# Kernel optimization log

Hardware: AMD Instinct MI355X
Metric: run time of the kernel (lower is better)

Reference implementation:

```python
import jax, jax.numpy as jnp
import numpy as np

EPS = 1e-3  # jitter to guarantee SPD input

def setup_inputs() -> dict:
    key = jax.random.key(0)
    B, N = 8192, 64
    a = jax.random.normal(key, (B, N, N), dtype=jnp.float32)
    # build batched SPD matrices: x = A A^T / N + eps I
    x = jnp.einsum('bij,bkj->bik', a, a) / N + EPS * jnp.eye(N, dtype=jnp.float32)
    return {"x": x}

def reference(x) -> jnp.ndarray:
    # LogEig: eigendecompose each SPD matrix, take log of eigenvalues,
    # reconstruct: U diag(log s) U^T
    w, v = jnp.linalg.eigh(x)                       # w: [B,N], v: [B,N,N]
    logw = jnp.log(w)
    # (v * logw[..., None, :]) scales columns of v by log-eigenvalues
    out = jnp.einsum('bik,bk,bjk->bij', v, logw, v)
    return out
```

## Files before the change

### kernel.cpp

```cpp
#include <hip/hip_runtime.h>
#include <math.h>

#define NTHR   512
#define SWEEPS 7

__device__ __forceinline__ int ring_next_even(int s) {
    return (s == 0) ? 0 : ((s == 62) ? 63 : s + 2);
}
__device__ __forceinline__ int ring_next_odd(int s) {
    return (s == 1) ? 2 : s - 2;
}
__device__ __forceinline__ int cpos(int c) {
    return (c >> 1) + ((c & 1) << 5);
}

__global__ __launch_bounds__(NTHR, 8)
void logeig_jacobi(const float* __restrict__ x, float* __restrict__ out) {
    __shared__ float A[64 * 64];
    __shared__ float Vt[64 * 64];
    __shared__ __align__(16) float2 prm[32];
    __shared__ float logw[64];

    const int tid = threadIdx.x;
    const int w   = tid >> 6;
    const int lan = tid & 63;
    const int J   = tid & 31;
    const int bit = (lan >> 5) & 1;
    const int base = 4 * w + bit;
    const int kv  = tid >> 4;
    const int cch = tid & 15;

    const int wpP = cpos(ring_next_even(2 * J));
    const int wpQ = cpos(ring_next_odd(2 * J + 1));

    const size_t base_el = (size_t)blockIdx.x * 4096;

    {
        const float4* x4 = (const float4*)(x + base_el);
        for (int idx4 = tid; idx4 < 1024; idx4 += NTHR) {
            int i = idx4 >> 4, t = idx4 & 15;
            float4 v = x4[idx4];
            *(float2*)&A[i * 64 + 2 * t]      = make_float2(v.x, v.z);
            *(float2*)&A[i * 64 + 32 + 2 * t] = make_float2(v.y, v.w);
            float4 id;
            id.x = (4 * t + 0 == i) ? 1.0f : 0.0f;
            id.y = (4 * t + 1 == i) ? 1.0f : 0.0f;
            id.z = (4 * t + 2 == i) ? 1.0f : 0.0f;
            id.w = (4 * t + 3 == i) ? 1.0f : 0.0f;
            ((float4*)Vt)[idx4] = id;
        }
    }
    __syncthreads();

    for (int sweep = 0; sweep < SWEEPS; ++sweep) {
        for (int r = 0; r < 63; ++r) {
            if (tid < 32) {
                int k = tid;
                float app = A[(2 * k) * 64 + k];
                float apq = A[(2 * k) * 64 + k + 32];
                float aqq = A[(2 * k + 1) * 64 + k + 32];
                float c = 1.0f, s = 0.0f;
                if (apq != 0.0f) {
                    float tau = (aqq - app) / (2.0f * apq);
                    float t   = copysignf(1.0f, tau) /
                                (fabsf(tau) + sqrtf(1.0f + tau * tau));
                    c = 1.0f / sqrtf(1.0f + t * t);
                    s = t * c;
                }
                prm[k] = make_float2(c, s);
            }

            float4 ablk[2];
            #pragma unroll
            for (int k = 0; k < 2; ++k) {
                int r0 = (2 * (base + 2 * k)) * 64;
                int r1 = r0 + 64;
                ablk[k] = make_float4(A[r0 + J], A[r0 + J + 32],
                                      A[r1 + J], A[r1 + J + 32]);
            }
            float4 vtop = *(const float4*)&Vt[(2 * kv) * 64 + 4 * cch];
            float4 vbot = *(const float4*)&Vt[(2 * kv + 1) * 64 + 4 * cch];
            __syncthreads();

            float2 pJ = prm[J];
            float2 pV = prm[kv];
            float2 pI[2];
            pI[0] = prm[base];
            pI[1] = prm[base + 2];

            #pragma unroll
            for (int k = 0; k < 2; ++k) {
                float cI = pI[k].x, sI = pI[k].y;
                float cJ = pJ.x,   sJ = pJ.y;
                float m00 = ablk[k].x, m01 = ablk[k].y;
                float m10 = ablk[k].z, m11 = ablk[k].w;
                float t00 = cI * m00 - sI * m10, t01 = cI * m01 - sI * m11;
                float t10 = sI * m00 + cI * m10, t11 = sI * m01 + cI * m11;
                float n00 = cJ * t00 - sJ * t01, n01 = sJ * t00 + cJ * t01;
                float n10 = cJ * t10 - sJ * t11, n11 = sJ * t10 + cJ * t11;
                int I  = base + 2 * k;
                int dPr = ring_next_even(2 * I) * 64;
                int dQr = ring_next_odd(2 * I + 1) * 64;
                A[dPr + wpP] = n00;
                A[dPr + wpQ] = n01;
                A[dQr + wpP] = n10;
                A[dQr + wpQ] = n11;
            }

            {
                float cV = pV.x, sV = pV.y;
                int dPr = ring_next_even(2 * kv);
                int dQr = ring_next_odd(2 * kv + 1);
                float4 n0, n1;
                n0.x = cV * vtop.x - sV * vbot.x;  n1.x = sV * vtop.x + cV * vbot.x;
                n0.y = cV * vtop.y - sV * vbot.y;  n1.y = sV * vtop.y + cV * vbot.y;
                n0.z = cV * vtop.z - sV * vbot.z;  n1.z = sV * vtop.z + cV * vbot.z;
                n0.w = cV * vtop.w - sV * vbot.w;  n1.w = sV * vtop.w + cV * vbot.w;
                *(float4*)&Vt[dPr * 64 + 4 * cch] = n0;
                *(float4*)&Vt[dQr * 64 + 4 * cch] = n1;
            }
            __syncthreads();
        }
    }

    if (tid < 64) {
        int p = (tid >> 1) + ((tid & 1) << 5);
        logw[tid] = logf(A[tid * 64 + p]);
    }
    __syncthreads();

    for (int idx4 = tid; idx4 < 1024; idx4 += NTHR) {
        int k = idx4 >> 4;
        float lw = logw[k];
        float4 v = ((float4*)Vt)[idx4];
        v.x *= lw; v.y *= lw; v.z *= lw; v.w *= lw;
        ((float4*)A)[idx4] = v;
    }
    __syncthreads();

    float4* out4 = (float4*)(out + base_el);
    for (int idx4 = tid; idx4 < 1024; idx4 += NTHR) {
        int i = idx4 >> 4, j4 = idx4 & 15;
        float4 acc = make_float4(0.0f, 0.0f, 0.0f, 0.0f);
        #pragma unroll 8
        for (int k = 0; k < 64; ++k) {
            float a = A[k * 64 + i];
            float4 vv = ((float4*)Vt)[k * 16 + j4];
            acc.x += a * vv.x; acc.y += a * vv.y;
            acc.z += a * vv.z; acc.w += a * vv.w;
        }
        out4[idx4] = acc;
    }
}

extern "C" void kernel_launch(void* const* d_in, const int* in_sizes, int n_in,
                              void* d_out, int out_size, void* d_ws, size_t ws_size,
                              hipStream_t stream) {
    const float* x = (const float*)d_in[0];
    float* o = (float*)d_out;
    int B = in_sizes[0] / 4096;
    logeig_jacobi<<<B, NTHR, 0, stream>>>(x, o);
}
```

Before: 5.044 ms.

## Exploit symmetry in Jacobi A update, computing only upper-triangle 2x2 blocks

Each thread now owns one off-diagonal 2x2 block pair (k,q) and writes both it and its transpose, cutting the A-rotation work per sweep step roughly in half (one block per thread instead of two). The diagonal blocks are written directly in closed form (app - t*apq, 0, 0, aqq + t*apq) by the parameter threads, which avoids rounding error in the zeroed entries. The cost is more scattered shared-memory stores per thread, possible bank conflicts, and some idle threads in the last half-warp group.

```diff
diff --git a/kernel.cpp b/kernel.cpp
--- a/kernel.cpp
+++ b/kernel.cpp
@@ -16,22 +16,40 @@
 
 __global__ __launch_bounds__(NTHR, 8)
 void logeig_jacobi(const float* __restrict__ x, float* __restrict__ out) {
-    __shared__ float A[64 * 64];
-    __shared__ float Vt[64 * 64];
+    __shared__ __align__(16) float A[64 * 64];
+    __shared__ __align__(16) float Vt[64 * 64];
     __shared__ __align__(16) float2 prm[32];
     __shared__ float logw[64];
 
     const int tid = threadIdx.x;
-    const int w   = tid >> 6;
-    const int lan = tid & 63;
-    const int J   = tid & 31;
-    const int bit = (lan >> 5) & 1;
-    const int base = 4 * w + bit;
+    const int k   = tid & 31;
+    const int hw  = tid >> 5;
+    const int d   = hw + 1;
+    const int q   = (k + d) & 31;
+    const bool act = (d < 16) || (k < 16);
+
+    const int ro00 = (2 * k) * 64 + q;
+
+    const int dRp = ring_next_even(2 * k);
+    const int dRq = ring_next_odd(2 * k + 1);
+    const int dCp = cpos(ring_next_even(2 * q));
+    const int dCq = cpos(ring_next_odd(2 * q + 1));
+    const int tRp = ring_next_even(2 * q);
+    const int tRq = ring_next_odd(2 * q + 1);
+    const int tCp = cpos(ring_next_even(2 * k));
+    const int tCq = cpos(ring_next_odd(2 * k + 1));
+
+    const int w00 = dRp * 64 + dCp, w01 = dRp * 64 + dCq;
+    const int w10 = dRq * 64 + dCp, w11 = dRq * 64 + dCq;
+    const int u00 = tRp * 64 + tCp, u01 = tRp * 64 + tCq;
+    const int u10 = tRq * 64 + tCp, u11 = tRq * 64 + tCq;
+    const int g00 = dRp * 64 + tCp, g01 = dRp * 64 + tCq;
+    const int g10 = dRq * 64 + tCp, g11 = dRq * 64 + tCq;
+
     const int kv  = tid >> 4;
     const int cch = tid & 15;
-
-    const int wpP = cpos(ring_next_even(2 * J));
-    const int wpQ = cpos(ring_next_odd(2 * J + 1));
+    const int vdP = ring_next_even(2 * kv);
+    const int vdQ = ring_next_odd(2 * kv + 1);
 
     const size_t base_el = (size_t)blockIdx.x * 4096;
 
@@ -54,70 +72,62 @@
 
     for (int sweep = 0; sweep < SWEEPS; ++sweep) {
         for (int r = 0; r < 63; ++r) {
+            float app = 0.0f, apq = 0.0f, aqq = 0.0f, tpar = 0.0f;
             if (tid < 32) {
-                int k = tid;
-                float app = A[(2 * k) * 64 + k];
-                float apq = A[(2 * k) * 64 + k + 32];
-                float aqq = A[(2 * k + 1) * 64 + k + 32];
+                app = A[(2 * k) * 64 + k];
+                apq = A[(2 * k) * 64 + 32 + k];
+                aqq = A[(2 * k + 1) * 64 + 32 + k];
                 float c = 1.0f, s = 0.0f;
                 if (apq != 0.0f) {
                     float tau = (aqq - app) / (2.0f * apq);
-                    float t   = copysignf(1.0f, tau) /
-                                (fabsf(tau) + sqrtf(1.0f + tau * tau));
-                    c = 1.0f / sqrtf(1.0f + t * t);
-                    s = t * c;
+                    tpar = copysignf(1.0f, tau) /
+                           (fabsf(tau) + sqrtf(1.0f + tau * tau));
+                    c = 1.0f / sqrtf(1.0f + tpar * tpar);
+                    s = tpar * c;
                 }
                 prm[k] = make_float2(c, s);
             }
 
-            float4 ablk[2];
-            #pragma unroll
-            for (int k = 0; k < 2; ++k) {
-                int r0 = (2 * (base + 2 * k)) * 64;
-                int r1 = r0 + 64;
-                ablk[k] = make_float4(A[r0 + J], A[r0 + J + 32],
-                                      A[r1 + J], A[r1 + J + 32]);
+            float m00 = 0.f, m01 = 0.f, m10 = 0.f, m11 = 0.f;
+            if (act) {
+                m00 = A[ro00];       m01 = A[ro00 + 32];
+                m10 = A[ro00 + 64];  m11 = A[ro00 + 96];
             }
             float4 vtop = *(const float4*)&Vt[(2 * kv) * 64 + 4 * cch];
             float4 vbot = *(const float4*)&Vt[(2 * kv + 1) * 64 + 4 * cch];
             __syncthreads();
 
-            float2 pJ = prm[J];
             float2 pV = prm[kv];
-            float2 pI[2];
-            pI[0] = prm[base];
-            pI[1] = prm[base + 2];
 
-            #pragma unroll
-            for (int k = 0; k < 2; ++k) {
-                float cI = pI[k].x, sI = pI[k].y;
-                float cJ = pJ.x,   sJ = pJ.y;
-                float m00 = ablk[k].x, m01 = ablk[k].y;
-                float m10 = ablk[k].z, m11 = ablk[k].w;
-                float t00 = cI * m00 - sI * m10, t01 = cI * m01 - sI * m11;
-                float t10 = sI * m00 + cI * m10, t11 = sI * m01 + cI * m11;
-                float n00 = cJ * t00 - sJ * t01, n01 = sJ * t00 + cJ * t01;
-                float n10 = cJ * t10 - sJ * t11, n11 = sJ * t10 + cJ * t11;
-                int I  = base + 2 * k;
-                int dPr = ring_next_even(2 * I) * 64;
-                int dQr = ring_next_odd(2 * I + 1) * 64;
-                A[dPr + wpP] = n00;
-                A[dPr + wpQ] = n01;
-                A[dQr + wpP] = n10;
-                A[dQr + wpQ] = n11;
+            if (act) {
+                float2 pP = prm[k];
+                float2 pQ = prm[q];
+                float cP = pP.x, sP = pP.y, cQ = pQ.x, sQ = pQ.y;
+                float t00 = cP * m00 - sP * m10, t01 = cP * m01 - sP * m11;
+                float t10 = sP * m00 + cP * m10, t11 = sP * m01 + cP * m11;
+                float n00 = cQ * t00 - sQ * t01, n01 = sQ * t00 + cQ * t01;
+                float n10 = cQ * t10 - sQ * t11, n11 = sQ * t10 + cQ * t11;
+                A[w00] = n00;  A[w01] = n01;
+                A[w10] = n10;  A[w11] = n11;
+                A[u00] = n00;  A[u01] = n10;
+                A[u10] = n01;  A[u11] = n11;
+            }
+            if (tid < 32) {
+                A[g00] = app - tpar * apq;
+                A[g01] = 0.0f;
+                A[g10] = 0.0f;
+                A[g11] = aqq + tpar * apq;
             }
 
             {
                 float cV = pV.x, sV = pV.y;
-                int dPr = ring_next_even(2 * kv);
-                int dQr = ring_next_odd(2 * kv + 1);
                 float4 n0, n1;
                 n0.x = cV * vtop.x - sV * vbot.x;  n1.x = sV * vtop.x + cV * vbot.x;
                 n0.y = cV * vtop.y - sV * vbot.y;  n1.y = sV * vtop.y + cV * vbot.y;
                 n0.z = cV * vtop.z - sV * vbot.z;  n1.z = sV * vtop.z + cV * vbot.z;
                 n0.w = cV * vtop.w - sV * vbot.w;  n1.w = sV * vtop.w + cV * vbot.w;
-                *(float4*)&Vt[dPr * 64 + 4 * cch] = n0;
-                *(float4*)&Vt[dQr * 64 + 4 * cch] = n1;
+                *(float4*)&Vt[vdP * 64 + 4 * cch] = n0;
+                *(float4*)&Vt[vdQ * 64 + 4 * cch] = n1;
             }
             __syncthreads();
         }
@@ -130,8 +140,8 @@
     __syncthreads();
 
     for (int idx4 = tid; idx4 < 1024; idx4 += NTHR) {
-        int k = idx4 >> 4;
-        float lw = logw[k];
+        int kk = idx4 >> 4;
+        float lw = logw[kk];
         float4 v = ((float4*)Vt)[idx4];
         v.x *= lw; v.y *= lw; v.z *= lw; v.w *= lw;
         ((float4*)A)[idx4] = v;
@@ -143,9 +153,9 @@
         int i = idx4 >> 4, j4 = idx4 & 15;
         float4 acc = make_float4(0.0f, 0.0f, 0.0f, 0.0f);
         #pragma unroll 8
-        for (int k = 0; k < 64; ++k) {
-            float a = A[k * 64 + i];
-            float4 vv = ((float4*)Vt)[k * 16 + j4];
+        for (int kk = 0; kk < 64; ++kk) {
+            float a = A[kk * 64 + i];
+            float4 vv = ((float4*)Vt)[kk * 16 + j4];
             acc.x += a * vv.x; acc.y += a * vv.y;
             acc.z += a * vv.z; acc.w += a * vv.w;
         }
```

New measurement: 4.599 ms. -8.8%, faster.
